# Performance work log

Measured on AMD Instinct MI355X. Metric: run time of the kernel, lower is better.

Reference implementation:

```python
import jax, jax.numpy as jnp
import numpy as np

N_NODES = 100000
N_EDGES = 1600000
D_FEAT = 64


def setup_inputs() -> dict:
    key = jax.random.key(0)
    k1, k2 = jax.random.split(key)
    x = jax.random.normal(k1, (N_NODES, D_FEAT), dtype=jnp.float32)
    edge_index = jax.random.randint(k2, (2, N_EDGES), 0, N_NODES, dtype=jnp.int64)
    return {"x": x, "edge_index": edge_index}


def reference(x, edge_index):
    # GCNProp (improved=False): remove self loops, add self loops w/ weight 1,
    # symmetric deg^-1/2 normalization, then spmm aggregation.
    N = x.shape[0]
    row, col = edge_index[0], edge_index[1]
    # remove_self_loops: zero the weight of any self-loop edge (math-equivalent
    # to dropping it, and jit-friendly: no data-dependent shapes).
    w = jnp.where(row != col, jnp.ones((), x.dtype), jnp.zeros((), x.dtype))
    # add_self_loops: append N diagonal edges with loop_value = 1 (improved=False)
    loop = jnp.arange(N, dtype=row.dtype)
    row_a = jnp.concatenate([row, loop])          # [E+N]
    col_a = jnp.concatenate([col, loop])          # [E+N]
    w_a = jnp.concatenate([w, jnp.ones((N,), x.dtype)])  # [E+N]
    # degree via scatter_add over rows
    deg = jax.ops.segment_sum(w_a, row_a, num_segments=N)  # [N]
    # deg^-0.5 with inf -> 0
    dinv = jnp.where(deg > 0, jax.lax.rsqrt(deg), jnp.zeros((), x.dtype))
    # edge normalization: deg[row]^-1/2 * w * deg[col]^-1/2
    norm = dinv[row_a] * w_a * dinv[col_a]        # [E+N]
    # spmm: gather neighbor features, scale, scatter-add into rows
    out = jax.ops.segment_sum(norm[:, None] * x[col_a], row_a, num_segments=N)  # [N, D]
    return out
```

## Files before the change

kernel.cpp:

```cpp
#include <hip/hip_runtime.h>

#define N_NODES 100000
#define N_EDGES 1600000
#define D 64
#define NB 391
#define BCAP 4480
#define PBLK 256
#define STPB 1024
#define TPB 512
#define CHUNK ((N_EDGES + PBLK - 1) / PBLK)
#define K_FULL (CHUNK / STPB)
#define K_REM (CHUNK - K_FULL * STPB)
#define CURSTRIDE 32
#define CROWS 64

typedef int iv4 __attribute__((ext_vector_type(4)));
typedef float fv4 __attribute__((ext_vector_type(4)));

__device__ __forceinline__ unsigned short f2b(float f) {
    unsigned u = __float_as_uint(f);
    u += 0x7FFF + ((u >> 16) & 1);
    return (unsigned short)(u >> 16);
}

__global__ __launch_bounds__(STPB) void scatter_direct_kernel(const int* __restrict__ ei,
                                                              int* __restrict__ cursor,
                                                              int* __restrict__ epack) {
    __shared__ int h[NB];
    __shared__ int lbase[NB];
    __shared__ int lcur[NB];
    int t = threadIdx.x;
    for (int i = t; i < NB; i += STPB) h[i] = 0;
    __syncthreads();
    int s = blockIdx.x * CHUNK + t;
    int r0 = __builtin_nontemporal_load(ei + s);
    int c0 = __builtin_nontemporal_load(ei + N_EDGES + s);
    int r1 = __builtin_nontemporal_load(ei + s + 1 * STPB);
    int c1 = __builtin_nontemporal_load(ei + N_EDGES + s + 1 * STPB);
    int r2 = __builtin_nontemporal_load(ei + s + 2 * STPB);
    int c2 = __builtin_nontemporal_load(ei + N_EDGES + s + 2 * STPB);
    int r3 = __builtin_nontemporal_load(ei + s + 3 * STPB);
    int c3 = __builtin_nontemporal_load(ei + N_EDGES + s + 3 * STPB);
    int r4 = __builtin_nontemporal_load(ei + s + 4 * STPB);
    int c4 = __builtin_nontemporal_load(ei + N_EDGES + s + 4 * STPB);
    int r5 = __builtin_nontemporal_load(ei + s + 5 * STPB);
    int c5 = __builtin_nontemporal_load(ei + N_EDGES + s + 5 * STPB);
    int r6 = 0, c6 = 0;
    if (t < K_REM) {
        r6 = __builtin_nontemporal_load(ei + s + 6 * STPB);
        c6 = __builtin_nontemporal_load(ei + N_EDGES + s + 6 * STPB);
    }
    if (r0 != c0) atomicAdd(&h[r0 >> 8], 1);
    if (r1 != c1) atomicAdd(&h[r1 >> 8], 1);
    if (r2 != c2) atomicAdd(&h[r2 >> 8], 1);
    if (r3 != c3) atomicAdd(&h[r3 >> 8], 1);
    if (r4 != c4) atomicAdd(&h[r4 >> 8], 1);
    if (r5 != c5) atomicAdd(&h[r5 >> 8], 1);
    if (r6 != c6) atomicAdd(&h[r6 >> 8], 1);
    __syncthreads();
    for (int i = t; i < NB; i += STPB) {
        int hv = h[i];
        lbase[i] = hv ? (i * BCAP + atomicAdd(&cursor[i * CURSTRIDE], hv)) : 0;
        lcur[i] = 0;
    }
    __syncthreads();
#define PUT_EDGE(rr, cc)                                            \
    if (rr != cc) {                                                 \
        int bb = rr >> 8;                                           \
        int p = lbase[bb] + atomicAdd(&lcur[bb], 1);                \
        epack[p] = ((rr & 255) << 17) | cc;                         \
    }
    PUT_EDGE(r0, c0)
    PUT_EDGE(r1, c1)
    PUT_EDGE(r2, c2)
    PUT_EDGE(r3, c3)
    PUT_EDGE(r4, c4)
    PUT_EDGE(r5, c5)
    PUT_EDGE(r6, c6)
#undef PUT_EDGE
}

__global__ __launch_bounds__(TPB) void csr_sort_kernel(const int* __restrict__ cursor,
                                                       const int* __restrict__ epack,
                                                       int* __restrict__ colsorted,
                                                       int2* __restrict__ rowinfo,
                                                       float* __restrict__ dinv) {
    __shared__ int h[256];
    __shared__ int cur[256];
    __shared__ int wtot[4];
    int b = blockIdx.x;
    int t = threadIdx.x;
    int base = b * BCAP;
    int n = min(cursor[b * CURSTRIDE], BCAP);
    if (t < 256) h[t] = 0;
    __syncthreads();
    const iv4* ep4 = (const iv4*)(epack + base);
    int n4 = n >> 2;
    for (int i = t; i < n4; i += TPB) {
        iv4 v = ep4[i];
        atomicAdd(&h[v.x >> 17], 1);
        atomicAdd(&h[v.y >> 17], 1);
        atomicAdd(&h[v.z >> 17], 1);
        atomicAdd(&h[v.w >> 17], 1);
    }
    for (int i = (n4 << 2) + t; i < n; i += TPB) {
        atomicAdd(&h[epack[base + i] >> 17], 1);
    }
    __syncthreads();
    int lane = t & 63;
    int w = t >> 6;
    int myh = (t < 256) ? h[t] : 0;
    int v = myh;
    for (int off = 1; off < 64; off <<= 1) {
        int u = __shfl_up(v, off);
        if (lane >= off) v += u;
    }
    if (t < 256 && lane == 63) wtot[w] = v;
    __syncthreads();
    if (t < 256) {
        int woff = 0;
        if (w > 0) woff += wtot[0];
        if (w > 1) woff += wtot[1];
        if (w > 2) woff += wtot[2];
        int incl = v + woff;
        int excl = incl - myh;
        int row = b * 256 + t;
        if (row < N_NODES) {
            rowinfo[row] = make_int2(base + excl, myh);
            dinv[row] = rsqrtf((float)(1 + myh));
        }
        cur[t] = excl;
    }
    __syncthreads();
    for (int i = t; i < n4; i += TPB) {
        iv4 v = ep4[i];
        int p0 = atomicAdd(&cur[v.x >> 17], 1);
        colsorted[base + p0] = (v.x & 0x1FFFF) << 7;
        int p1 = atomicAdd(&cur[v.y >> 17], 1);
        colsorted[base + p1] = (v.y & 0x1FFFF) << 7;
        int p2 = atomicAdd(&cur[v.z >> 17], 1);
        colsorted[base + p2] = (v.z & 0x1FFFF) << 7;
        int p3 = atomicAdd(&cur[v.w >> 17], 1);
        colsorted[base + p3] = (v.w & 0x1FFFF) << 7;
    }
    for (int i = (n4 << 2) + t; i < n; i += TPB) {
        int p = epack[base + i];
        int pos = atomicAdd(&cur[p >> 17], 1);
        colsorted[base + pos] = (p & 0x1FFFF) << 7;
    }
}

__global__ __launch_bounds__(256) void convert_kernel(const float* __restrict__ x,
                                                      const float* __restrict__ dinv,
                                                      unsigned short* __restrict__ xs) {
    __shared__ float dv[CROWS];
    int b = blockIdx.x;
    int t = threadIdx.x;
    int r0 = b * CROWS;
    int nrows = min(CROWS, N_NODES - r0);
    if (t < nrows) dv[t] = dinv[r0 + t];
    __syncthreads();
    const fv4* x4 = (const fv4*)x;
    ushort4* xs4 = (ushort4*)xs;
    for (int i = t; i < nrows * 16; i += 256) {
        int rl = i >> 4;
        fv4 vv = __builtin_nontemporal_load(x4 + (size_t)(r0 + rl) * 16 + (i & 15));
        float dd = dv[rl];
        ushort4 o;
        o.x = f2b(vv.x * dd);
        o.y = f2b(vv.y * dd);
        o.z = f2b(vv.z * dd);
        o.w = f2b(vv.w * dd);
        xs4[(size_t)(r0 + rl) * 16 + (i & 15)] = o;
    }
}

__global__ __launch_bounds__(256) void gather_kernel(const unsigned short* __restrict__ xs,
                                                     const int2* __restrict__ rowinfo,
                                                     const int* __restrict__ colidx,
                                                     float* __restrict__ out) {
    int t = blockIdx.x * blockDim.x + threadIdx.x;
    int r = t >> 6;
    int lane = t & 63;
    if (r >= N_NODES) return;
    int lp = lane & 31;
    int hf = lane >> 5;
    int lpo = lp << 2;
    int2 ri = rowinfo[r];
    int start = ri.x;
    int end = start + ri.y;
    float dr = rsqrtf((float)(1 + ri.y));
    const char* xsb = (const char*)xs;
    float ax = 0.0f, ay = 0.0f;
    if (hf == 0) {
        unsigned v = *(const unsigned*)(xsb + (((size_t)r) << 7) + lpo);
        ax = __uint_as_float(v << 16);
        ay = __uint_as_float(v & 0xFFFF0000u);
    }
    for (int j = start; j < end; j += 64) {
        int idx = j + lane;
        int cj = (idx < end) ? colidx[idx] : 0;
        int n = min(64, end - j);
        int k = 0;
        for (; 2 * (k + 8) <= n; k += 8) {
            int s0 = __shfl(cj, 2 * k + hf);
            int s1 = __shfl(cj, 2 * k + 2 + hf);
            int s2 = __shfl(cj, 2 * k + 4 + hf);
            int s3 = __shfl(cj, 2 * k + 6 + hf);
            int s4 = __shfl(cj, 2 * k + 8 + hf);
            int s5 = __shfl(cj, 2 * k + 10 + hf);
            int s6 = __shfl(cj, 2 * k + 12 + hf);
            int s7 = __shfl(cj, 2 * k + 14 + hf);
            unsigned v0 = *(const unsigned*)(xsb + (unsigned)(s0 + lpo));
            unsigned v1 = *(const unsigned*)(xsb + (unsigned)(s1 + lpo));
            unsigned v2 = *(const unsigned*)(xsb + (unsigned)(s2 + lpo));
            unsigned v3 = *(const unsigned*)(xsb + (unsigned)(s3 + lpo));
            unsigned v4 = *(const unsigned*)(xsb + (unsigned)(s4 + lpo));
            unsigned v5 = *(const unsigned*)(xsb + (unsigned)(s5 + lpo));
            unsigned v6 = *(const unsigned*)(xsb + (unsigned)(s6 + lpo));
            unsigned v7 = *(const unsigned*)(xsb + (unsigned)(s7 + lpo));
            float a0 = __uint_as_float(v0 << 16), b0 = __uint_as_float(v0 & 0xFFFF0000u);
            float a1 = __uint_as_float(v1 << 16), b1 = __uint_as_float(v1 & 0xFFFF0000u);
            float a2 = __uint_as_float(v2 << 16), b2 = __uint_as_float(v2 & 0xFFFF0000u);
            float a3 = __uint_as_float(v3 << 16), b3 = __uint_as_float(v3 & 0xFFFF0000u);
            float a4 = __uint_as_float(v4 << 16), b4 = __uint_as_float(v4 & 0xFFFF0000u);
            float a5 = __uint_as_float(v5 << 16), b5 = __uint_as_float(v5 & 0xFFFF0000u);
            float a6 = __uint_as_float(v6 << 16), b6 = __uint_as_float(v6 & 0xFFFF0000u);
            float a7 = __uint_as_float(v7 << 16), b7 = __uint_as_float(v7 & 0xFFFF0000u);
            ax += ((a0 + a1) + (a2 + a3)) + ((a4 + a5) + (a6 + a7));
            ay += ((b0 + b1) + (b2 + b3)) + ((b4 + b5) + (b6 + b7));
        }
        for (; 2 * (k + 4) <= n; k += 4) {
            int s0 = __shfl(cj, 2 * k + hf);
            int s1 = __shfl(cj, 2 * k + 2 + hf);
            int s2 = __shfl(cj, 2 * k + 4 + hf);
            int s3 = __shfl(cj, 2 * k + 6 + hf);
            unsigned v0 = *(const unsigned*)(xsb + (unsigned)(s0 + lpo));
            unsigned v1 = *(const unsigned*)(xsb + (unsigned)(s1 + lpo));
            unsigned v2 = *(const unsigned*)(xsb + (unsigned)(s2 + lpo));
            unsigned v3 = *(const unsigned*)(xsb + (unsigned)(s3 + lpo));
            float a0 = __uint_as_float(v0 << 16), b0 = __uint_as_float(v0 & 0xFFFF0000u);
            float a1 = __uint_as_float(v1 << 16), b1 = __uint_as_float(v1 & 0xFFFF0000u);
            float a2 = __uint_as_float(v2 << 16), b2 = __uint_as_float(v2 & 0xFFFF0000u);
            float a3 = __uint_as_float(v3 << 16), b3 = __uint_as_float(v3 & 0xFFFF0000u);
            ax += (a0 + a1) + (a2 + a3);
            ay += (b0 + b1) + (b2 + b3);
        }
        for (; 2 * k < n; k++) {
            int src = 2 * k + hf;
            int s0 = __shfl(cj, (src < n) ? src : (n - 1));
            unsigned v0 = *(const unsigned*)(xsb + (unsigned)(s0 + lpo));
            if (src < n) {
                ax += __uint_as_float(v0 << 16);
                ay += __uint_as_float(v0 & 0xFFFF0000u);
            }
        }
    }
    ax += __shfl_xor(ax, 32);
    ay += __shfl_xor(ay, 32);
    if (hf == 0) {
        float2 o;
        o.x = dr * ax;
        o.y = dr * ay;
        ((float2*)out)[(size_t)r * 32 + lp] = o;
    }
}

extern "C" void kernel_launch(void* const* d_in, const int* in_sizes, int n_in,
                              void* d_out, int out_size, void* d_ws, size_t ws_size,
                              hipStream_t stream) {
    const float* x = (const float*)d_in[0];
    const int* ei = (const int*)d_in[1];
    float* out = (float*)d_out;

    int* cursor = (int*)d_ws;
    int2* rowinfo = (int2*)(cursor + NB * CURSTRIDE);
    float* dinv = (float*)(rowinfo + N_NODES);
    int* epack = (int*)(dinv + N_NODES);
    int* colsorted = epack + NB * BCAP;
    unsigned short* xs = (unsigned short*)(colsorted + NB * BCAP);

    (void)hipMemsetAsync(cursor, 0, NB * CURSTRIDE * sizeof(int), stream);
    scatter_direct_kernel<<<PBLK, STPB, 0, stream>>>(ei, cursor, epack);
    csr_sort_kernel<<<NB, TPB, 0, stream>>>(cursor, epack, colsorted, rowinfo, dinv);
    convert_kernel<<<(N_NODES + CROWS - 1) / CROWS, 256, 0, stream>>>(x, dinv, xs);
    gather_kernel<<<(N_NODES * D + 255) / 256, 256, 0, stream>>>(xs, rowinfo, colsorted, out);
}
```

Baseline: 151.9 us.

## Fuse memset, scatter, CSR sort and convert into one cooperative kernel

Replaces the memset plus three preprocessing kernels with a single cooperative-launch kernel that uses grid-wide syncs between phases. The bucket sort and the bf16 conversion of x now run in the same per-bucket loop, and dinv stays in shared memory instead of a global buffer. This removes several launch gaps and a global round trip for dinv. In exchange it adds grid.sync overhead, runs the sort phase with only 256 blocks over 391 buckets (so some blocks handle two), and depends on cooperative launch residency.

Result: slower. 223.3 us (+47.0%).

```diff
diff --git a/kernel.cpp b/kernel.cpp
--- a/kernel.cpp
+++ b/kernel.cpp
@@ -1,18 +1,19 @@
 #include <hip/hip_runtime.h>
+#include <hip/hip_cooperative_groups.h>
+
+namespace cg = cooperative_groups;
 
 #define N_NODES 100000
 #define N_EDGES 1600000
 #define D 64
 #define NB 391
 #define BCAP 4480
-#define PBLK 256
-#define STPB 1024
-#define TPB 512
-#define CHUNK ((N_EDGES + PBLK - 1) / PBLK)
-#define K_FULL (CHUNK / STPB)
-#define K_REM (CHUNK - K_FULL * STPB)
+#define GRID 256
+#define MTPB 1024
+#define CHUNK ((N_EDGES + GRID - 1) / GRID)
+#define K_FULL (CHUNK / MTPB)
+#define K_REM (CHUNK - K_FULL * MTPB)
 #define CURSTRIDE 32
-#define CROWS 64
 
 typedef int iv4 __attribute__((ext_vector_type(4)));
 typedef float fv4 __attribute__((ext_vector_type(4)));
@@ -23,32 +24,47 @@
     return (unsigned short)(u >> 16);
 }
 
-__global__ __launch_bounds__(STPB) void scatter_direct_kernel(const int* __restrict__ ei,
-                                                              int* __restrict__ cursor,
-                                                              int* __restrict__ epack) {
+__global__ __launch_bounds__(MTPB) void preproc_kernel(const int* __restrict__ ei,
+                                                       int* __restrict__ cursor,
+                                                       int* __restrict__ epack,
+                                                       int* __restrict__ colsorted,
+                                                       int2* __restrict__ rowinfo,
+                                                       const float* __restrict__ x,
+                                                       unsigned short* __restrict__ xs) {
     __shared__ int h[NB];
     __shared__ int lbase[NB];
     __shared__ int lcur[NB];
+    __shared__ int hs[256];
+    __shared__ int cur[256];
+    __shared__ float dv[256];
+    __shared__ int wtot[16];
+    cg::grid_group grid = cg::this_grid();
     int t = threadIdx.x;
-    for (int i = t; i < NB; i += STPB) h[i] = 0;
+    int bid = blockIdx.x;
+
+    int gtid = bid * MTPB + t;
+    if (gtid < NB) cursor[gtid * CURSTRIDE] = 0;
+    grid.sync();
+
+    for (int i = t; i < NB; i += MTPB) h[i] = 0;
     __syncthreads();
-    int s = blockIdx.x * CHUNK + t;
+    int s = bid * CHUNK + t;
     int r0 = __builtin_nontemporal_load(ei + s);
     int c0 = __builtin_nontemporal_load(ei + N_EDGES + s);
-    int r1 = __builtin_nontemporal_load(ei + s + 1 * STPB);
-    int c1 = __builtin_nontemporal_load(ei + N_EDGES + s + 1 * STPB);
-    int r2 = __builtin_nontemporal_load(ei + s + 2 * STPB);
-    int c2 = __builtin_nontemporal_load(ei + N_EDGES + s + 2 * STPB);
-    int r3 = __builtin_nontemporal_load(ei + s + 3 * STPB);
-    int c3 = __builtin_nontemporal_load(ei + N_EDGES + s + 3 * STPB);
-    int r4 = __builtin_nontemporal_load(ei + s + 4 * STPB);
-    int c4 = __builtin_nontemporal_load(ei + N_EDGES + s + 4 * STPB);
-    int r5 = __builtin_nontemporal_load(ei + s + 5 * STPB);
-    int c5 = __builtin_nontemporal_load(ei + N_EDGES + s + 5 * STPB);
+    int r1 = __builtin_nontemporal_load(ei + s + 1 * MTPB);
+    int c1 = __builtin_nontemporal_load(ei + N_EDGES + s + 1 * MTPB);
+    int r2 = __builtin_nontemporal_load(ei + s + 2 * MTPB);
+    int c2 = __builtin_nontemporal_load(ei + N_EDGES + s + 2 * MTPB);
+    int r3 = __builtin_nontemporal_load(ei + s + 3 * MTPB);
+    int c3 = __builtin_nontemporal_load(ei + N_EDGES + s + 3 * MTPB);
+    int r4 = __builtin_nontemporal_load(ei + s + 4 * MTPB);
+    int c4 = __builtin_nontemporal_load(ei + N_EDGES + s + 4 * MTPB);
+    int r5 = __builtin_nontemporal_load(ei + s + 5 * MTPB);
+    int c5 = __builtin_nontemporal_load(ei + N_EDGES + s + 5 * MTPB);
     int r6 = 0, c6 = 0;
     if (t < K_REM) {
-        r6 = __builtin_nontemporal_load(ei + s + 6 * STPB);
-        c6 = __builtin_nontemporal_load(ei + N_EDGES + s + 6 * STPB);
+        r6 = __builtin_nontemporal_load(ei + s + 6 * MTPB);
+        c6 = __builtin_nontemporal_load(ei + N_EDGES + s + 6 * MTPB);
     }
     if (r0 != c0) atomicAdd(&h[r0 >> 8], 1);
     if (r1 != c1) atomicAdd(&h[r1 >> 8], 1);
@@ -58,7 +74,7 @@
     if (r5 != c5) atomicAdd(&h[r5 >> 8], 1);
     if (r6 != c6) atomicAdd(&h[r6 >> 8], 1);
     __syncthreads();
-    for (int i = t; i < NB; i += STPB) {
+    for (int i = t; i < NB; i += MTPB) {
         int hv = h[i];
         lbase[i] = hv ? (i * BCAP + atomicAdd(&cursor[i * CURSTRIDE], hv)) : 0;
         lcur[i] = 0;
@@ -78,100 +94,79 @@
     PUT_EDGE(r5, c5)
     PUT_EDGE(r6, c6)
 #undef PUT_EDGE
-}
-
-__global__ __launch_bounds__(TPB) void csr_sort_kernel(const int* __restrict__ cursor,
-                                                       const int* __restrict__ epack,
-                                                       int* __restrict__ colsorted,
-                                                       int2* __restrict__ rowinfo,
-                                                       float* __restrict__ dinv) {
-    __shared__ int h[256];
-    __shared__ int cur[256];
-    __shared__ int wtot[4];
-    int b = blockIdx.x;
-    int t = threadIdx.x;
-    int base = b * BCAP;
-    int n = min(cursor[b * CURSTRIDE], BCAP);
-    if (t < 256) h[t] = 0;
-    __syncthreads();
-    const iv4* ep4 = (const iv4*)(epack + base);
-    int n4 = n >> 2;
-    for (int i = t; i < n4; i += TPB) {
-        iv4 v = ep4[i];
-        atomicAdd(&h[v.x >> 17], 1);
-        atomicAdd(&h[v.y >> 17], 1);
-        atomicAdd(&h[v.z >> 17], 1);
-        atomicAdd(&h[v.w >> 17], 1);
-    }
-    for (int i = (n4 << 2) + t; i < n; i += TPB) {
-        atomicAdd(&h[epack[base + i] >> 17], 1);
-    }
-    __syncthreads();
+    grid.sync();
+
     int lane = t & 63;
     int w = t >> 6;
-    int myh = (t < 256) ? h[t] : 0;
-    int v = myh;
-    for (int off = 1; off < 64; off <<= 1) {
-        int u = __shfl_up(v, off);
-        if (lane >= off) v += u;
-    }
-    if (t < 256 && lane == 63) wtot[w] = v;
-    __syncthreads();
-    if (t < 256) {
-        int woff = 0;
-        if (w > 0) woff += wtot[0];
-        if (w > 1) woff += wtot[1];
-        if (w > 2) woff += wtot[2];
-        int incl = v + woff;
-        int excl = incl - myh;
-        int row = b * 256 + t;
-        if (row < N_NODES) {
-            rowinfo[row] = make_int2(base + excl, myh);
-            dinv[row] = rsqrtf((float)(1 + myh));
-        }
-        cur[t] = excl;
-    }
-    __syncthreads();
-    for (int i = t; i < n4; i += TPB) {
-        iv4 v = ep4[i];
-        int p0 = atomicAdd(&cur[v.x >> 17], 1);
-        colsorted[base + p0] = (v.x & 0x1FFFF) << 7;
-        int p1 = atomicAdd(&cur[v.y >> 17], 1);
-        colsorted[base + p1] = (v.y & 0x1FFFF) << 7;
-        int p2 = atomicAdd(&cur[v.z >> 17], 1);
-        colsorted[base + p2] = (v.z & 0x1FFFF) << 7;
-        int p3 = atomicAdd(&cur[v.w >> 17], 1);
-        colsorted[base + p3] = (v.w & 0x1FFFF) << 7;
-    }
-    for (int i = (n4 << 2) + t; i < n; i += TPB) {
-        int p = epack[base + i];
-        int pos = atomicAdd(&cur[p >> 17], 1);
-        colsorted[base + pos] = (p & 0x1FFFF) << 7;
-    }
-}
-
-__global__ __launch_bounds__(256) void convert_kernel(const float* __restrict__ x,
-                                                      const float* __restrict__ dinv,
-                                                      unsigned short* __restrict__ xs) {
-    __shared__ float dv[CROWS];
-    int b = blockIdx.x;
-    int t = threadIdx.x;
-    int r0 = b * CROWS;
-    int nrows = min(CROWS, N_NODES - r0);
-    if (t < nrows) dv[t] = dinv[r0 + t];
-    __syncthreads();
-    const fv4* x4 = (const fv4*)x;
-    ushort4* xs4 = (ushort4*)xs;
-    for (int i = t; i < nrows * 16; i += 256) {
-        int rl = i >> 4;
-        fv4 vv = __builtin_nontemporal_load(x4 + (size_t)(r0 + rl) * 16 + (i & 15));
-        float dd = dv[rl];
-        ushort4 o;
-        o.x = f2b(vv.x * dd);
-        o.y = f2b(vv.y * dd);
-        o.z = f2b(vv.z * dd);
-        o.w = f2b(vv.w * dd);
-        xs4[(size_t)(r0 + rl) * 16 + (i & 15)] = o;
+    for (int b = bid; b < NB; b += GRID) {
+        __syncthreads();
+        if (t < 256) hs[t] = 0;
+        __syncthreads();
+        int base = b * BCAP;
+        int n = min(cursor[b * CURSTRIDE], BCAP);
+        const iv4* ep4 = (const iv4*)(epack + base);
+        int n4 = n >> 2;
+        for (int i = t; i < n4; i += MTPB) {
+            iv4 v = ep4[i];
+            atomicAdd(&hs[v.x >> 17], 1);
+            atomicAdd(&hs[v.y >> 17], 1);
+            atomicAdd(&hs[v.z >> 17], 1);
+            atomicAdd(&hs[v.w >> 17], 1);
+        }
+        for (int i = (n4 << 2) + t; i < n; i += MTPB) {
+            atomicAdd(&hs[epack[base + i] >> 17], 1);
+        }
+        __syncthreads();
+        int myh = (t < 256) ? hs[t] : 0;
+        int v = myh;
+        for (int off = 1; off < 64; off <<= 1) {
+            int u = __shfl_up(v, off);
+            if (lane >= off) v += u;
+        }
+        if (t < 256 && lane == 63) wtot[w] = v;
+        __syncthreads();
+        if (t < 256) {
+            int woff = 0;
+            if (w > 0) woff += wtot[0];
+            if (w > 1) woff += wtot[1];
+            if (w > 2) woff += wtot[2];
+            int excl = v + woff - myh;
+            int row = b * 256 + t;
+            if (row < N_NODES) rowinfo[row] = make_int2(base + excl, myh);
+            dv[t] = rsqrtf((float)(1 + myh));
+            cur[t] = excl;
+        }
+        __syncthreads();
+        for (int i = t; i < n4; i += MTPB) {
+            iv4 v4 = ep4[i];
+            int p0 = atomicAdd(&cur[v4.x >> 17], 1);
+            colsorted[base + p0] = (v4.x & 0x1FFFF) << 7;
+            int p1 = atomicAdd(&cur[v4.y >> 17], 1);
+            colsorted[base + p1] = (v4.y & 0x1FFFF) << 7;
+            int p2 = atomicAdd(&cur[v4.z >> 17], 1);
+            colsorted[base + p2] = (v4.z & 0x1FFFF) << 7;
+            int p3 = atomicAdd(&cur[v4.w >> 17], 1);
+            colsorted[base + p3] = (v4.w & 0x1FFFF) << 7;
+        }
+        for (int i = (n4 << 2) + t; i < n; i += MTPB) {
+            int p = epack[base + i];
+            int pos = atomicAdd(&cur[p >> 17], 1);
+            colsorted[base + pos] = (p & 0x1FFFF) << 7;
+        }
+        int nrows = min(256, N_NODES - b * 256);
+        const fv4* x4 = (const fv4*)x;
+        ushort4* xs4 = (ushort4*)xs;
+        for (int i = t; i < nrows * 16; i += MTPB) {
+            int rl = i >> 4;
+            fv4 vv = __builtin_nontemporal_load(x4 + (size_t)(b * 256 + rl) * 16 + (i & 15));
+            float dd = dv[rl];
+            ushort4 o;
+            o.x = f2b(vv.x * dd);
+            o.y = f2b(vv.y * dd);
+            o.z = f2b(vv.z * dd);
+            o.w = f2b(vv.w * dd);
+            xs4[(size_t)(b * 256 + rl) * 16 + (i & 15)] = o;
+        }
     }
 }
 
@@ -275,14 +270,13 @@
 
     int* cursor = (int*)d_ws;
     int2* rowinfo = (int2*)(cursor + NB * CURSTRIDE);
-    float* dinv = (float*)(rowinfo + N_NODES);
-    int* epack = (int*)(dinv + N_NODES);
+    int* epack = (int*)(rowinfo + N_NODES);
     int* colsorted = epack + NB * BCAP;
     unsigned short* xs = (unsigned short*)(colsorted + NB * BCAP);
 
-    (void)hipMemsetAsync(cursor, 0, NB * CURSTRIDE * sizeof(int), stream);
-    scatter_direct_kernel<<<PBLK, STPB, 0, stream>>>(ei, cursor, epack);
-    csr_sort_kernel<<<NB, TPB, 0, stream>>>(cursor, epack, colsorted, rowinfo, dinv);
-    convert_kernel<<<(N_NODES + CROWS - 1) / CROWS, 256, 0, stream>>>(x, dinv, xs);
+    void* args[] = {(void*)&ei, (void*)&cursor, (void*)&epack, (void*)&colsorted,
+                    (void*)&rowinfo, (void*)&x, (void*)&xs};
+    (void)hipLaunchCooperativeKernel((void*)preproc_kernel, dim3(GRID), dim3(MTPB),
+                                     args, 0, stream);
     gather_kernel<<<(N_NODES * D + 255) / 256, 256, 0, stream>>>(xs, rowinfo, colsorted, out);
 }
```
